# Kernel optimization log

Hardware: AMD Instinct MI355X
Metric: run time of the kernel (lower is better)

The kernel has to match this reference:

```python
import jax, jax.numpy as jnp
import numpy as np

N, E = 50000, 1600000
FEAT, HID, HEADS = 256, 64, 2
NEG_SLOPE = 0.2


def gat_conv(x, src, dst, W, att_src, att_dst, bias, heads, out_ch):
    """PyG GATConv (concat=True, self-loops already appended to src/dst)."""
    n = x.shape[0]
    h = (x @ W).reshape(n, heads, out_ch)                      # [N,H,C]
    a_src = jnp.einsum('nhc,hc->nh', h, att_src)               # [N,H]
    a_dst = jnp.einsum('nhc,hc->nh', h, att_dst)               # [N,H]
    alpha = jax.nn.leaky_relu(a_src[src] + a_dst[dst], NEG_SLOPE)  # [E',H]
    # segment softmax over incoming edges of each dst node
    amax = jax.ops.segment_max(alpha, dst, num_segments=n)
    alpha = jnp.exp(alpha - amax[dst])
    denom = jax.ops.segment_sum(alpha, dst, num_segments=n)
    alpha = alpha / (denom[dst] + 1e-16)
    msg = h[src] * alpha[..., None]                            # [E',H,C]
    out = jax.ops.segment_sum(msg, dst, num_segments=n)        # [N,H,C]
    return out.reshape(n, heads * out_ch) + bias


def setup_inputs() -> dict:
    key = jax.random.key(0)
    ks = jax.random.split(key, 10)
    x = jax.random.normal(ks[0], (N, FEAT), dtype=jnp.float32)
    edge_index = jax.random.randint(ks[1], (2, E), 0, N, dtype=jnp.int64)
    s1 = 1.0 / np.sqrt(FEAT)
    s2 = 1.0 / np.sqrt(HID * HEADS)
    sa = 1.0 / np.sqrt(HID)
    return {
        'x': x,
        'edge_index': edge_index,
        'W1': jax.random.uniform(ks[2], (FEAT, HEADS * HID), jnp.float32, -s1, s1),
        'att_src1': jax.random.uniform(ks[3], (HEADS, HID), jnp.float32, -sa, sa),
        'att_dst1': jax.random.uniform(ks[4], (HEADS, HID), jnp.float32, -sa, sa),
        'b1': jnp.zeros((HEADS * HID,), jnp.float32),
        'W2': jax.random.uniform(ks[5], (HEADS * HID, HID), jnp.float32, -s2, s2),
        'att_src2': jax.random.uniform(ks[6], (1, HID), jnp.float32, -sa, sa),
        'att_dst2': jax.random.uniform(ks[7], (1, HID), jnp.float32, -sa, sa),
        'b2': jnp.zeros((HID,), jnp.float32),
    }


def reference(x, edge_index, W1, att_src1, att_dst1, b1, W2, att_src2, att_dst2, b2):
    n = x.shape[0]
    loop = jnp.arange(n, dtype=edge_index.dtype)
    src = jnp.concatenate([edge_index[0], loop])   # add self loops (PyG default)
    dst = jnp.concatenate([edge_index[1], loop])
    h = gat_conv(x, src, dst, W1, att_src1, att_dst1, b1, HEADS, HID)
    h = jax.nn.relu(h)  # dropout is identity in eval mode
    h = gat_conv(h, src, dst, W2, att_src2, att_dst2, b2, 1, HID)
    return jax.nn.log_softmax(h, axis=1)
```

## Files before the change

kernel.cpp:

```cpp
#include <hip/hip_runtime.h>
#include <hip/hip_bf16.h>
#include <math.h>

typedef short bf16x8 __attribute__((ext_vector_type(8)));
typedef float f32x4 __attribute__((ext_vector_type(4)));

#define BSHIFT 7
#define BWIDTH 128
#define PCHUNK 8192

__global__ void prep_kernel(int* __restrict__ bcnt,
                            const float* __restrict__ W1, const float* __restrict__ W2,
                            __hip_bfloat16* __restrict__ W1t,
                            __hip_bfloat16* __restrict__ W2t) {
    if (blockIdx.x == 0) {
        bcnt[threadIdx.x] = 0;
        bcnt[threadIdx.x + 256] = 0;
        return;
    }
    int idx = (blockIdx.x - 1) * 256 + threadIdx.x;
    const int n1 = 128 * 256;
    if (idx < n1) {
        int nn = idx >> 8, kk = idx & 255;
        W1t[idx] = __float2bfloat16(W1[kk * 128 + nn]);
    } else {
        int j = idx - n1;
        if (j < 64 * 128) {
            int nn = j >> 7, kk = j & 127;
            W2t[j] = __float2bfloat16(W2[kk * 64 + nn]);
        }
    }
}

__global__ __launch_bounds__(256) void bucket_hist(const int* __restrict__ ei, int E,
                                                   int* __restrict__ bcnt) {
    __shared__ int h[512];
    int tid = threadIdx.x;
    for (int i = tid; i < 512; i += 256) h[i] = 0;
    __syncthreads();
    int start = blockIdx.x * PCHUNK;
    int cnt = min(PCHUNK, E - start);
    for (int i = tid; i < cnt; i += 256)
        atomicAdd(&h[ei[E + start + i] >> BSHIFT], 1);
    __syncthreads();
    for (int i = tid; i < 512; i += 256)
        if (h[i]) atomicAdd(&bcnt[i], h[i]);
}

__global__ __launch_bounds__(512) void bucket_scan(const int* __restrict__ bcnt,
                                                   int* __restrict__ bbase,
                                                   int* __restrict__ bcur,
                                                   int nbk, int n) {
    __shared__ int s[512];
    int tid = threadIdx.x;
    int nodes = 0;
    if (tid < nbk) nodes = min(BWIDTH, n - (tid << BSHIFT));
    int v = (tid < nbk) ? bcnt[tid] + nodes : 0;
    s[tid] = v;
    __syncthreads();
    #pragma unroll
    for (int o = 1; o < 512; o <<= 1) {
        int t = (tid >= o) ? s[tid - o] : 0;
        __syncthreads();
        s[tid] += t;
        __syncthreads();
    }
    if (tid < nbk) {
        int ex = s[tid] - v;
        bbase[tid] = ex;
        bcur[tid] = ex - (tid << BSHIFT);
    }
    if (tid == nbk) bbase[nbk] = s[tid];
}

__global__ __launch_bounds__(256) void partition_edges(const int* __restrict__ ei, int E,
                                                       int* __restrict__ bcur,
                                                       int* __restrict__ tmp) {
    __shared__ int stage[PCHUNK];
    __shared__ int h[512];
    __shared__ int lbase[512];
    int tid = threadIdx.x;
    int start = blockIdx.x * PCHUNK;
    int cnt = min(PCHUNK, E - start);
    for (int i = tid; i < 512; i += 256) h[i] = 0;
    __syncthreads();
    for (int i = tid; i < cnt; i += 256) {
        int s = ei[start + i];
        int d = ei[E + start + i];
        stage[i] = (s << 16) | d;
        atomicAdd(&h[d >> BSHIFT], 1);
    }
    __syncthreads();
    for (int i = tid; i < 512; i += 256) {
        if (h[i] > 0) lbase[i] = atomicAdd(&bcur[i], h[i]);
        h[i] = 0;
    }
    __syncthreads();
    for (int i = tid; i < cnt; i += 256) {
        int e = stage[i];
        int b = (e & 0xffff) >> BSHIFT;
        int r = atomicAdd(&h[b], 1);
        tmp[lbase[b] + r] = e;
    }
}

__global__ __launch_bounds__(256) void bucket_csr(const int* __restrict__ bbase,
                                                  const int* __restrict__ tmp,
                                                  int* __restrict__ offs,
                                                  int* __restrict__ srcs,
                                                  int n, int nbk) {
    __shared__ int cnt[BWIDTH];
    __shared__ int sa[BWIDTH];
    __shared__ int cur[BWIDTH];
    int b = blockIdx.x;
    int tid = threadIdx.x;
    int node0 = b << BSHIFT;
    int nnodes = min(BWIDTH, n - node0);
    int cb = bbase[b];
    int ce = bbase[b + 1];
    int tb = cb - node0;
    int ecnt = (ce - cb) - nnodes;

    if (tid < BWIDTH) cnt[tid] = (tid < nnodes) ? 1 : 0;
    __syncthreads();
    for (int i = tid; i < ecnt; i += 256)
        atomicAdd(&cnt[tmp[tb + i] & (BWIDTH - 1)], 1);
    __syncthreads();
    if (tid < BWIDTH) sa[tid] = cnt[tid];
    __syncthreads();
    #pragma unroll
    for (int o = 1; o < BWIDTH; o <<= 1) {
        int v = 0;
        if (tid < BWIDTH) { v = sa[tid]; if (tid >= o) v += sa[tid - o]; }
        __syncthreads();
        if (tid < BWIDTH) sa[tid] = v;
        __syncthreads();
    }
    if (tid < BWIDTH) {
        int ex = sa[tid] - cnt[tid];
        if (tid < nnodes) {
            offs[node0 + tid] = cb + ex;
            srcs[cb + ex] = node0 + tid;
        }
        cur[tid] = ex + (tid < nnodes ? 1 : 0);
    }
    if (b == nbk - 1 && tid == 0) offs[n] = ce;
    __syncthreads();
    for (int i = tid; i < ecnt; i += 256) {
        int e = tmp[tb + i];
        int li = e & (BWIDTH - 1);
        int r = atomicAdd(&cur[li], 1);
        srcs[cb + r] = ((unsigned)e) >> 16;
    }
}

template <bool A_BF16, int NT, int HEADS>
__global__ __launch_bounds__(256) void gemm_att(
    const void* __restrict__ Av, const __hip_bfloat16* __restrict__ Bt,
    __hip_bfloat16* __restrict__ C,
    const float* __restrict__ atts, const float* __restrict__ attd,
    float* __restrict__ a_s, float* __restrict__ a_d, int M, int K) {
    constexpr int N = NT * 16;
    __shared__ __hip_bfloat16 As[64][40];
    int tid = threadIdx.x;
    int w = tid >> 6, l = tid & 63;
    int q = l >> 4, m16 = l & 15;
    int bm = blockIdx.x * 64;

    int lr = tid >> 2, lseg = tid & 3;
    int arow = bm + lr; if (arow >= M) arow = M - 1;

    f32x4 acc[NT];
    #pragma unroll
    for (int t = 0; t < NT; t++) acc[t] = (f32x4){0.f, 0.f, 0.f, 0.f};

    for (int kc = 0; kc < K; kc += 32) {
        if (A_BF16) {
            const __hip_bfloat16* A = (const __hip_bfloat16*)Av;
            uint4 v = *(const uint4*)(A + (size_t)arow * K + kc + lseg * 8);
            *(uint4*)&As[lr][lseg * 8] = v;
        } else {
            const float* A = (const float*)Av;
            float4 v0 = *(const float4*)(A + (size_t)arow * K + kc + lseg * 8);
            float4 v1 = *(const float4*)(A + (size_t)arow * K + kc + lseg * 8 + 4);
            union { __hip_bfloat16 h[8]; uint4 u; } tmp;
            tmp.h[0] = __float2bfloat16(v0.x); tmp.h[1] = __float2bfloat16(v0.y);
            tmp.h[2] = __float2bfloat16(v0.z); tmp.h[3] = __float2bfloat16(v0.w);
            tmp.h[4] = __float2bfloat16(v1.x); tmp.h[5] = __float2bfloat16(v1.y);
            tmp.h[6] = __float2bfloat16(v1.z); tmp.h[7] = __float2bfloat16(v1.w);
            *(uint4*)&As[lr][lseg * 8] = tmp.u;
        }
        __syncthreads();
        bf16x8 a = *(const bf16x8*)&As[w * 16 + m16][q * 8];
        #pragma unroll
        for (int t = 0; t < NT; t++) {
            bf16x8 b = *(const bf16x8*)(Bt + (size_t)(t * 16 + m16) * K + kc + q * 8);
            acc[t] = __builtin_amdgcn_mfma_f32_16x16x32_bf16(a, b, acc[t], 0, 0, 0);
        }
        __syncthreads();
    }

    #pragma unroll
    for (int t = 0; t < NT; t++) {
        #pragma unroll
        for (int r = 0; r < 4; r++) {
            int row = bm + w * 16 + q * 4 + r;
            if (row < M) C[(size_t)row * N + t * 16 + m16] = __float2bfloat16(acc[t][r]);
        }
    }

    float ps[HEADS][4], pd[HEADS][4];
    #pragma unroll
    for (int hh = 0; hh < HEADS; hh++)
        #pragma unroll
        for (int r = 0; r < 4; r++) { ps[hh][r] = 0.f; pd[hh][r] = 0.f; }
    #pragma unroll
    for (int t = 0; t < NT; t++) {
        int ch = t * 16 + m16;
        float asw = atts[ch], adw = attd[ch];
        int hh = (HEADS == 2) ? (t >> 2) : 0;
        #pragma unroll
        for (int r = 0; r < 4; r++) {
            ps[hh][r] = fmaf(acc[t][r], asw, ps[hh][r]);
            pd[hh][r] = fmaf(acc[t][r], adw, pd[hh][r]);
        }
    }
    #pragma unroll
    for (int o = 1; o < 16; o <<= 1) {
        #pragma unroll
        for (int hh = 0; hh < HEADS; hh++)
            #pragma unroll
            for (int r = 0; r < 4; r++) {
                ps[hh][r] += __shfl_xor(ps[hh][r], o);
                pd[hh][r] += __shfl_xor(pd[hh][r], o);
            }
    }
    if (m16 == 0) {
        #pragma unroll
        for (int r = 0; r < 4; r++) {
            int row = bm + w * 16 + q * 4 + r;
            if (row < M) {
                if (HEADS == 2) {
                    a_s[row * 2]     = ps[0][r];
                    a_s[row * 2 + 1] = ps[1][r];
                    a_d[row * 2]     = pd[0][r];
                    a_d[row * 2 + 1] = pd[1][r];
                } else {
                    a_s[row] = ps[0][r];
                    a_d[row] = pd[0][r];
                }
            }
        }
    }
}

__device__ __forceinline__ float leaky(float r) {
    return r < 0.f ? 0.2f * r : r;
}

__device__ __forceinline__ void unpack2(unsigned u, float& lo, float& hi) {
    lo = __uint_as_float(u << 16);
    hi = __uint_as_float(u & 0xffff0000u);
}

__global__ __launch_bounds__(256) void edge_agg_l1(
    const int* __restrict__ offs, const int* __restrict__ srcs,
    const __hip_bfloat16* __restrict__ h1, const float* __restrict__ asv,
    const float* __restrict__ adv, const float* __restrict__ bias,
    __hip_bfloat16* __restrict__ out, int n) {
    int d = (blockIdx.x * blockDim.x + threadIdx.x) >> 6;
    int lane = threadIdx.x & 63;
    if (d >= n) return;
    int start = offs[d], end = offs[d + 1];
    float ad0 = adv[2 * d], ad1 = adv[2 * d + 1];

    int sub = lane & 15;
    int g = lane >> 4;
    int ch0 = sub * 8;
    int hsel = sub >> 3;

    float s0 = 0.f, s1 = 0.f;
    float acc[8];
    #pragma unroll
    for (int k = 0; k < 8; k++) acc[k] = 0.f;

    for (int base = start; base < end; base += 64) {
        int cnt = min(64, end - base);
        int s_l = 0;
        float e0 = 0.f, e1 = 0.f;
        if (lane < cnt) {
            s_l = srcs[base + lane];
            float2 a = *(const float2*)(asv + 2 * s_l);
            e0 = __expf(leaky(a.x + ad0));
            e1 = __expf(leaky(a.y + ad1));
        }
        s0 += e0;
        s1 += e1;

        int steps = (cnt + 3) >> 2;
        int jj = 0;
        for (; jj + 2 <= steps; jj += 2) {
            int eA = jj * 4 + g, eB = eA + 4;
            float w0A = __shfl(e0, eA), w1A = __shfl(e1, eA);
            int sA = __shfl(s_l, eA);
            float w0B = __shfl(e0, eB), w1B = __shfl(e1, eB);
            int sB = __shfl(s_l, eB);
            float wA = hsel ? w1A : w0A;
            float wB = hsel ? w1B : w0B;
            uint4 vA = *(const uint4*)(h1 + (size_t)sA * 128 + ch0);
            uint4 vB = *(const uint4*)(h1 + (size_t)sB * 128 + ch0);
            float f0, f1, f2, f3, f4, f5, f6, f7;
            unpack2(vA.x, f0, f1); unpack2(vA.y, f2, f3);
            unpack2(vA.z, f4, f5); unpack2(vA.w, f6, f7);
            acc[0] = fmaf(wA, f0, acc[0]); acc[1] = fmaf(wA, f1, acc[1]);
            acc[2] = fmaf(wA, f2, acc[2]); acc[3] = fmaf(wA, f3, acc[3]);
            acc[4] = fmaf(wA, f4, acc[4]); acc[5] = fmaf(wA, f5, acc[5]);
            acc[6] = fmaf(wA, f6, acc[6]); acc[7] = fmaf(wA, f7, acc[7]);
            unpack2(vB.x, f0, f1); unpack2(vB.y, f2, f3);
            unpack2(vB.z, f4, f5); unpack2(vB.w, f6, f7);
            acc[0] = fmaf(wB, f0, acc[0]); acc[1] = fmaf(wB, f1, acc[1]);
            acc[2] = fmaf(wB, f2, acc[2]); acc[3] = fmaf(wB, f3, acc[3]);
            acc[4] = fmaf(wB, f4, acc[4]); acc[5] = fmaf(wB, f5, acc[5]);
            acc[6] = fmaf(wB, f6, acc[6]); acc[7] = fmaf(wB, f7, acc[7]);
        }
        if (jj < steps) {
            int eA = jj * 4 + g;
            float w0A = __shfl(e0, eA), w1A = __shfl(e1, eA);
            int sA = __shfl(s_l, eA);
            float wA = hsel ? w1A : w0A;
            uint4 vA = *(const uint4*)(h1 + (size_t)sA * 128 + ch0);
            float f0, f1, f2, f3, f4, f5, f6, f7;
            unpack2(vA.x, f0, f1); unpack2(vA.y, f2, f3);
            unpack2(vA.z, f4, f5); unpack2(vA.w, f6, f7);
            acc[0] = fmaf(wA, f0, acc[0]); acc[1] = fmaf(wA, f1, acc[1]);
            acc[2] = fmaf(wA, f2, acc[2]); acc[3] = fmaf(wA, f3, acc[3]);
            acc[4] = fmaf(wA, f4, acc[4]); acc[5] = fmaf(wA, f5, acc[5]);
            acc[6] = fmaf(wA, f6, acc[6]); acc[7] = fmaf(wA, f7, acc[7]);
        }
    }
    #pragma unroll
    for (int o = 16; o < 64; o <<= 1)
        #pragma unroll
        for (int k = 0; k < 8; k++) acc[k] += __shfl_xor(acc[k], o);
    #pragma unroll
    for (int o = 1; o < 64; o <<= 1) {
        s0 += __shfl_xor(s0, o);
        s1 += __shfl_xor(s1, o);
    }

    if (lane < 16) {
        float invh = 1.f / ((hsel ? s1 : s0) + 1e-16f);
        float4 b0 = *(const float4*)(bias + ch0);
        float4 b1 = *(const float4*)(bias + ch0 + 4);
        union { __hip_bfloat16 h[8]; uint4 u; } o2;
        o2.h[0] = __float2bfloat16(fmaxf(fmaf(acc[0], invh, b0.x), 0.f));
        o2.h[1] = __float2bfloat16(fmaxf(fmaf(acc[1], invh, b0.y), 0.f));
        o2.h[2] = __float2bfloat16(fmaxf(fmaf(acc[2], invh, b0.z), 0.f));
        o2.h[3] = __float2bfloat16(fmaxf(fmaf(acc[3], invh, b0.w), 0.f));
        o2.h[4] = __float2bfloat16(fmaxf(fmaf(acc[4], invh, b1.x), 0.f));
        o2.h[5] = __float2bfloat16(fmaxf(fmaf(acc[5], invh, b1.y), 0.f));
        o2.h[6] = __float2bfloat16(fmaxf(fmaf(acc[6], invh, b1.z), 0.f));
        o2.h[7] = __float2bfloat16(fmaxf(fmaf(acc[7], invh, b1.w), 0.f));
        *(uint4*)(out + (size_t)d * 128 + ch0) = o2.u;
    }
}

__global__ __launch_bounds__(256) void edge_agg_l2(
    const int* __restrict__ offs, const int* __restrict__ srcs,
    const __hip_bfloat16* __restrict__ h2, const float* __restrict__ asv,
    const float* __restrict__ adv, const float* __restrict__ bias,
    float* __restrict__ out, int n) {
    int d = (blockIdx.x * blockDim.x + threadIdx.x) >> 6;
    int lane = threadIdx.x & 63;
    if (d >= n) return;
    int start = offs[d], end = offs[d + 1];
    float ad = adv[d];

    int sub = lane & 7;
    int g = lane >> 3;
    int ch0 = sub * 8;

    float ssum = 0.f;
    float acc[8];
    #pragma unroll
    for (int k = 0; k < 8; k++) acc[k] = 0.f;

    for (int base = start; base < end; base += 64) {
        int cnt = min(64, end - base);
        int s_l = 0;
        float ew = 0.f;
        if (lane < cnt) {
            s_l = srcs[base + lane];
            ew = __expf(leaky(asv[s_l] + ad));
        }
        ssum += ew;

        int steps = (cnt + 7) >> 3;
        int jj = 0;
        for (; jj + 2 <= steps; jj += 2) {
            int eA = jj * 8 + g, eB = eA + 8;
            float wA = __shfl(ew, eA);
            int sA = __shfl(s_l, eA);
            float wB = __shfl(ew, eB);
            int sB = __shfl(s_l, eB);
            uint4 vA = *(const uint4*)(h2 + (size_t)sA * 64 + ch0);
            uint4 vB = *(const uint4*)(h2 + (size_t)sB * 64 + ch0);
            float f0, f1, f2, f3, f4, f5, f6, f7;
            unpack2(vA.x, f0, f1); unpack2(vA.y, f2, f3);
            unpack2(vA.z, f4, f5); unpack2(vA.w, f6, f7);
            acc[0] = fmaf(wA, f0, acc[0]); acc[1] = fmaf(wA, f1, acc[1]);
            acc[2] = fmaf(wA, f2, acc[2]); acc[3] = fmaf(wA, f3, acc[3]);
            acc[4] = fmaf(wA, f4, acc[4]); acc[5] = fmaf(wA, f5, acc[5]);
            acc[6] = fmaf(wA, f6, acc[6]); acc[7] = fmaf(wA, f7, acc[7]);
            unpack2(vB.x, f0, f1); unpack2(vB.y, f2, f3);
            unpack2(vB.z, f4, f5); unpack2(vB.w, f6, f7);
            acc[0] = fmaf(wB, f0, acc[0]); acc[1] = fmaf(wB, f1, acc[1]);
            acc[2] = fmaf(wB, f2, acc[2]); acc[3] = fmaf(wB, f3, acc[3]);
            acc[4] = fmaf(wB, f4, acc[4]); acc[5] = fmaf(wB, f5, acc[5]);
            acc[6] = fmaf(wB, f6, acc[6]); acc[7] = fmaf(wB, f7, acc[7]);
        }
        if (jj < steps) {
            int eA = jj * 8 + g;
            float wA = __shfl(ew, eA);
            int sA = __shfl(s_l, eA);
            uint4 vA = *(const uint4*)(h2 + (size_t)sA * 64 + ch0);
            float f0, f1, f2, f3, f4, f5, f6, f7;
            unpack2(vA.x, f0, f1); unpack2(vA.y, f2, f3);
            unpack2(vA.z, f4, f5); unpack2(vA.w, f6, f7);
            acc[0] = fmaf(wA, f0, acc[0]); acc[1] = fmaf(wA, f1, acc[1]);
            acc[2] = fmaf(wA, f2, acc[2]); acc[3] = fmaf(wA, f3, acc[3]);
            acc[4] = fmaf(wA, f4, acc[4]); acc[5] = fmaf(wA, f5, acc[5]);
            acc[6] = fmaf(wA, f6, acc[6]); acc[7] = fmaf(wA, f7, acc[7]);
        }
    }
    #pragma unroll
    for (int o = 8; o < 64; o <<= 1)
        #pragma unroll
        for (int k = 0; k < 8; k++) acc[k] += __shfl_xor(acc[k], o);
    #pragma unroll
    for (int o = 1; o < 64; o <<= 1) ssum += __shfl_xor(ssum, o);

    float inv = 1.f / (ssum + 1e-16f);
    float4 b0 = *(const float4*)(bias + ch0);
    float4 b1 = *(const float4*)(bias + ch0 + 4);
    float v[8];
    v[0] = fmaf(acc[0], inv, b0.x); v[1] = fmaf(acc[1], inv, b0.y);
    v[2] = fmaf(acc[2], inv, b0.z); v[3] = fmaf(acc[3], inv, b0.w);
    v[4] = fmaf(acc[4], inv, b1.x); v[5] = fmaf(acc[5], inv, b1.y);
    v[6] = fmaf(acc[6], inv, b1.z); v[7] = fmaf(acc[7], inv, b1.w);

    float vm = v[0];
    #pragma unroll
    for (int k = 1; k < 8; k++) vm = fmaxf(vm, v[k]);
    #pragma unroll
    for (int o = 1; o < 8; o <<= 1) vm = fmaxf(vm, __shfl_xor(vm, o));
    float se_loc = 0.f;
    #pragma unroll
    for (int k = 0; k < 8; k++) se_loc += __expf(v[k] - vm);
    #pragma unroll
    for (int o = 1; o < 8; o <<= 1) se_loc += __shfl_xor(se_loc, o);
    float lse = vm + logf(se_loc);

    if (lane < 8) {
        float4 o0 = make_float4(v[0] - lse, v[1] - lse, v[2] - lse, v[3] - lse);
        float4 o1 = make_float4(v[4] - lse, v[5] - lse, v[6] - lse, v[7] - lse);
        *(float4*)(out + (size_t)d * 64 + ch0) = o0;
        *(float4*)(out + (size_t)d * 64 + ch0 + 4) = o1;
    }
}

extern "C" void kernel_launch(void* const* d_in, const int* in_sizes, int n_in,
                              void* d_out, int out_size, void* d_ws, size_t ws_size,
                              hipStream_t stream) {
    const float* x    = (const float*)d_in[0];
    const int*   ei   = (const int*)d_in[1];
    const float* W1   = (const float*)d_in[2];
    const float* as1w = (const float*)d_in[3];
    const float* ad1w = (const float*)d_in[4];
    const float* b1   = (const float*)d_in[5];
    const float* W2   = (const float*)d_in[6];
    const float* as2w = (const float*)d_in[7];
    const float* ad2w = (const float*)d_in[8];
    const float* b2   = (const float*)d_in[9];
    float* out = (float*)d_out;

    const int n = in_sizes[0] / 256;
    const int E = in_sizes[1] / 2;
    const int tot = E + n;
    const int nbk = (n + BWIDTH - 1) / BWIDTH;

    char* p = (char*)d_ws;
    auto alloc = [&](size_t bytes) {
        void* r = (void*)p;
        p += (bytes + 255) & ~(size_t)255;
        return r;
    };
    int*   offs  = (int*)alloc((size_t)(n + 1) * 4);
    int*   srcs  = (int*)alloc((size_t)tot * 4);
    int*   tmp   = (int*)alloc((size_t)E * 4);
    int*   bcnt  = (int*)alloc(512 * 4);
    int*   bbase = (int*)alloc(512 * 4);
    int*   bcur  = (int*)alloc(512 * 4);
    __hip_bfloat16* W1t = (__hip_bfloat16*)alloc((size_t)128 * 256 * 2);
    __hip_bfloat16* W2t = (__hip_bfloat16*)alloc((size_t)64 * 128 * 2);
    __hip_bfloat16* h1  = (__hip_bfloat16*)alloc((size_t)n * 128 * 2);
    __hip_bfloat16* out1= (__hip_bfloat16*)alloc((size_t)n * 128 * 2);
    __hip_bfloat16* h2  = (__hip_bfloat16*)alloc((size_t)n * 64 * 2);
    float* a_s1 = (float*)alloc((size_t)n * 2 * 4);
    float* a_d1 = (float*)alloc((size_t)n * 2 * 4);
    float* a_s2 = (float*)alloc((size_t)n * 4);
    float* a_d2 = (float*)alloc((size_t)n * 4);

    int pblocks = (E + PCHUNK - 1) / PCHUNK;

    prep_kernel<<<1 + (128 * 256 + 64 * 128 + 255) / 256, 256, 0, stream>>>(
        bcnt, W1, W2, W1t, W2t);

    bucket_hist<<<pblocks, 256, 0, stream>>>(ei, E, bcnt);
    bucket_scan<<<1, 512, 0, stream>>>(bcnt, bbase, bcur, nbk, n);
    partition_edges<<<pblocks, 256, 0, stream>>>(ei, E, bcur, tmp);
    bucket_csr<<<nbk, 256, 0, stream>>>(bbase, tmp, offs, srcs, n, nbk);

    gemm_att<false, 8, 2><<<(n + 63) / 64, 256, 0, stream>>>(
        x, W1t, h1, as1w, ad1w, a_s1, a_d1, n, 256);
    edge_agg_l1<<<((size_t)n * 64 + 255) / 256, 256, 0, stream>>>(
        offs, srcs, h1, a_s1, a_d1, b1, out1, n);

    gemm_att<true, 4, 1><<<(n + 63) / 64, 256, 0, stream>>>(
        out1, W2t, h2, as2w, ad2w, a_s2, a_d2, n, 128);
    edge_agg_l2<<<((size_t)n * 64 + 255) / 256, 256, 0, stream>>>(
        offs, srcs, h2, a_s2, a_d2, b2, out, n);
}
```

Before: 286.5 us.

## Fuse CSR build pipeline into one cooperative kernel with grid syncs

Replaces the prep, histogram, scan, partition and per-bucket CSR kernels with a single cooperative kernel separated by grid.sync barriers. Each block stages its edge chunk in LDS once and reuses it for both the histogram and the partition phases, so edges are read from global memory only once. Every block redundantly computes the bucket scan, and the weight transpose is folded into the same kernel. PCHUNK is halved so the grid covers both edges and buckets, with launch bounds chosen so all blocks stay co-resident. The cost is grid-wide barrier latency and a dependence on co-residency for the cooperative launch.

New measurement: 435.6 us. +52.0%, slower.

```diff
diff --git a/kernel.cpp b/kernel.cpp
--- a/kernel.cpp
+++ b/kernel.cpp
@@ -1,156 +1,142 @@
 #include <hip/hip_runtime.h>
 #include <hip/hip_bf16.h>
+#include <hip/hip_cooperative_groups.h>
 #include <math.h>
+
+namespace cg = cooperative_groups;
 
 typedef short bf16x8 __attribute__((ext_vector_type(8)));
 typedef float f32x4 __attribute__((ext_vector_type(4)));
 
 #define BSHIFT 7
 #define BWIDTH 128
-#define PCHUNK 8192
-
-__global__ void prep_kernel(int* __restrict__ bcnt,
-                            const float* __restrict__ W1, const float* __restrict__ W2,
-                            __hip_bfloat16* __restrict__ W1t,
-                            __hip_bfloat16* __restrict__ W2t) {
-    if (blockIdx.x == 0) {
-        bcnt[threadIdx.x] = 0;
-        bcnt[threadIdx.x + 256] = 0;
-        return;
-    }
-    int idx = (blockIdx.x - 1) * 256 + threadIdx.x;
-    const int n1 = 128 * 256;
-    if (idx < n1) {
-        int nn = idx >> 8, kk = idx & 255;
-        W1t[idx] = __float2bfloat16(W1[kk * 128 + nn]);
-    } else {
-        int j = idx - n1;
-        if (j < 64 * 128) {
-            int nn = j >> 7, kk = j & 127;
-            W2t[j] = __float2bfloat16(W2[kk * 64 + nn]);
-        }
-    }
-}
-
-__global__ __launch_bounds__(256) void bucket_hist(const int* __restrict__ ei, int E,
-                                                   int* __restrict__ bcnt) {
+#define PCHUNK 4096
+
+__global__ __launch_bounds__(256, 2) void build_coop(
+    const int* __restrict__ ei, int E,
+    const float* __restrict__ W1, const float* __restrict__ W2,
+    __hip_bfloat16* __restrict__ W1t, __hip_bfloat16* __restrict__ W2t,
+    int* __restrict__ bcnt, int* __restrict__ bcur, int* __restrict__ tmp,
+    int* __restrict__ offs, int* __restrict__ srcs, int n, int nbk) {
+    cg::grid_group grid = cg::this_grid();
+    __shared__ int stage[PCHUNK];
     __shared__ int h[512];
-    int tid = threadIdx.x;
+    __shared__ int aux[512];
+    __shared__ int bb[513];
+    int b = blockIdx.x, tid = threadIdx.x;
+    int nblk = gridDim.x;
+
     for (int i = tid; i < 512; i += 256) h[i] = 0;
     __syncthreads();
-    int start = blockIdx.x * PCHUNK;
-    int cnt = min(PCHUNK, E - start);
-    for (int i = tid; i < cnt; i += 256)
-        atomicAdd(&h[ei[E + start + i] >> BSHIFT], 1);
-    __syncthreads();
-    for (int i = tid; i < 512; i += 256)
-        if (h[i]) atomicAdd(&bcnt[i], h[i]);
-}
-
-__global__ __launch_bounds__(512) void bucket_scan(const int* __restrict__ bcnt,
-                                                   int* __restrict__ bbase,
-                                                   int* __restrict__ bcur,
-                                                   int nbk, int n) {
-    __shared__ int s[512];
-    int tid = threadIdx.x;
-    int nodes = 0;
-    if (tid < nbk) nodes = min(BWIDTH, n - (tid << BSHIFT));
-    int v = (tid < nbk) ? bcnt[tid] + nodes : 0;
-    s[tid] = v;
-    __syncthreads();
-    #pragma unroll
-    for (int o = 1; o < 512; o <<= 1) {
-        int t = (tid >= o) ? s[tid - o] : 0;
-        __syncthreads();
-        s[tid] += t;
-        __syncthreads();
-    }
-    if (tid < nbk) {
-        int ex = s[tid] - v;
-        bbase[tid] = ex;
-        bcur[tid] = ex - (tid << BSHIFT);
-    }
-    if (tid == nbk) bbase[nbk] = s[tid];
-}
-
-__global__ __launch_bounds__(256) void partition_edges(const int* __restrict__ ei, int E,
-                                                       int* __restrict__ bcur,
-                                                       int* __restrict__ tmp) {
-    __shared__ int stage[PCHUNK];
-    __shared__ int h[512];
-    __shared__ int lbase[512];
-    int tid = threadIdx.x;
-    int start = blockIdx.x * PCHUNK;
-    int cnt = min(PCHUNK, E - start);
-    for (int i = tid; i < 512; i += 256) h[i] = 0;
-    __syncthreads();
+    int start = b * PCHUNK;
+    int cnt = E - start;
+    cnt = cnt < 0 ? 0 : (cnt > PCHUNK ? PCHUNK : cnt);
     for (int i = tid; i < cnt; i += 256) {
         int s = ei[start + i];
         int d = ei[E + start + i];
         stage[i] = (s << 16) | d;
         atomicAdd(&h[d >> BSHIFT], 1);
     }
+    {
+        const int TW = 128 * 256 + 64 * 128;
+        for (int idx = b * 256 + tid; idx < TW; idx += nblk * 256) {
+            if (idx < 128 * 256) {
+                int nn = idx >> 8, kk = idx & 255;
+                W1t[idx] = __float2bfloat16(W1[kk * 128 + nn]);
+            } else {
+                int j = idx - 128 * 256;
+                int nn = j >> 7, kk = j & 127;
+                W2t[j] = __float2bfloat16(W2[kk * 64 + nn]);
+            }
+        }
+    }
     __syncthreads();
-    for (int i = tid; i < 512; i += 256) {
-        if (h[i] > 0) lbase[i] = atomicAdd(&bcur[i], h[i]);
-        h[i] = 0;
-    }
-    __syncthreads();
-    for (int i = tid; i < cnt; i += 256) {
-        int e = stage[i];
-        int b = (e & 0xffff) >> BSHIFT;
-        int r = atomicAdd(&h[b], 1);
-        tmp[lbase[b] + r] = e;
-    }
-}
-
-__global__ __launch_bounds__(256) void bucket_csr(const int* __restrict__ bbase,
-                                                  const int* __restrict__ tmp,
-                                                  int* __restrict__ offs,
-                                                  int* __restrict__ srcs,
-                                                  int n, int nbk) {
-    __shared__ int cnt[BWIDTH];
-    __shared__ int sa[BWIDTH];
-    __shared__ int cur[BWIDTH];
-    int b = blockIdx.x;
-    int tid = threadIdx.x;
-    int node0 = b << BSHIFT;
-    int nnodes = min(BWIDTH, n - node0);
-    int cb = bbase[b];
-    int ce = bbase[b + 1];
-    int tb = cb - node0;
-    int ecnt = (ce - cb) - nnodes;
-
-    if (tid < BWIDTH) cnt[tid] = (tid < nnodes) ? 1 : 0;
-    __syncthreads();
-    for (int i = tid; i < ecnt; i += 256)
-        atomicAdd(&cnt[tmp[tb + i] & (BWIDTH - 1)], 1);
-    __syncthreads();
-    if (tid < BWIDTH) sa[tid] = cnt[tid];
-    __syncthreads();
-    #pragma unroll
-    for (int o = 1; o < BWIDTH; o <<= 1) {
-        int v = 0;
-        if (tid < BWIDTH) { v = sa[tid]; if (tid >= o) v += sa[tid - o]; }
-        __syncthreads();
-        if (tid < BWIDTH) sa[tid] = v;
-        __syncthreads();
-    }
-    if (tid < BWIDTH) {
-        int ex = sa[tid] - cnt[tid];
-        if (tid < nnodes) {
-            offs[node0 + tid] = cb + ex;
-            srcs[cb + ex] = node0 + tid;
-        }
-        cur[tid] = ex + (tid < nnodes ? 1 : 0);
-    }
-    if (b == nbk - 1 && tid == 0) offs[n] = ce;
-    __syncthreads();
-    for (int i = tid; i < ecnt; i += 256) {
-        int e = tmp[tb + i];
-        int li = e & (BWIDTH - 1);
-        int r = atomicAdd(&cur[li], 1);
-        srcs[cb + r] = ((unsigned)e) >> 16;
+    for (int i = tid; i < 512; i += 256)
+        if (h[i]) atomicAdd(&bcnt[i], h[i]);
+    grid.sync();
+
+    {
+        int j0 = 2 * tid, j1 = 2 * tid + 1;
+        int nodes0 = (j0 < nbk) ? min(BWIDTH, n - (j0 << BSHIFT)) : 0;
+        int nodes1 = (j1 < nbk) ? min(BWIDTH, n - (j1 << BSHIFT)) : 0;
+        int v0 = bcnt[j0] + nodes0;
+        int v1 = bcnt[j1] + nodes1;
+        int psum = v0 + v1;
+        aux[tid] = psum;
+        __syncthreads();
+        #pragma unroll
+        for (int o = 1; o < 256; o <<= 1) {
+            int add = (tid >= o) ? aux[tid - o] : 0;
+            __syncthreads();
+            aux[tid] += add;
+            __syncthreads();
+        }
+        int incl = aux[tid];
+        int excl = incl - psum;
+        bb[j0] = excl;
+        bb[j1] = excl + v0;
+        if (tid == 255) bb[512] = incl;
+        __syncthreads();
+        if (tid == 0 && b < nbk) bcur[b] = bb[b] - (b << BSHIFT);
+        if (b == nbk - 1 && tid == 0) offs[n] = bb[nbk];
+    }
+    grid.sync();
+
+    {
+        for (int i = tid; i < 512; i += 256) {
+            int c = h[i];
+            aux[i] = (c > 0) ? atomicAdd(&bcur[i], c) : 0;
+            h[i] = 0;
+        }
+        __syncthreads();
+        for (int i = tid; i < cnt; i += 256) {
+            int e = stage[i];
+            int bkt = (e & 0xffff) >> BSHIFT;
+            int r = atomicAdd(&h[bkt], 1);
+            tmp[aux[bkt] + r] = e;
+        }
+    }
+    grid.sync();
+
+    if (b < nbk) {
+        int* cnt128 = h;
+        int* sa = h + 128;
+        int* cur = h + 256;
+        int node0 = b << BSHIFT;
+        int nnodes = min(BWIDTH, n - node0);
+        int cb = bb[b], ce = bb[b + 1];
+        int tb = cb - node0;
+        int ecnt = (ce - cb) - nnodes;
+        if (tid < BWIDTH) cnt128[tid] = (tid < nnodes) ? 1 : 0;
+        __syncthreads();
+        for (int i = tid; i < ecnt; i += 256)
+            atomicAdd(&cnt128[tmp[tb + i] & (BWIDTH - 1)], 1);
+        __syncthreads();
+        if (tid < BWIDTH) sa[tid] = cnt128[tid];
+        __syncthreads();
+        #pragma unroll
+        for (int o = 1; o < BWIDTH; o <<= 1) {
+            int v = 0;
+            if (tid < BWIDTH) { v = sa[tid]; if (tid >= o) v += sa[tid - o]; }
+            __syncthreads();
+            if (tid < BWIDTH) sa[tid] = v;
+            __syncthreads();
+        }
+        if (tid < BWIDTH) {
+            int ex = sa[tid] - cnt128[tid];
+            if (tid < nnodes) {
+                offs[node0 + tid] = cb + ex;
+                srcs[cb + ex] = node0 + tid;
+            }
+            cur[tid] = ex + (tid < nnodes ? 1 : 0);
+        }
+        __syncthreads();
+        for (int i = tid; i < ecnt; i += 256) {
+            int e = tmp[tb + i];
+            int li = e & (BWIDTH - 1);
+            int r = atomicAdd(&cur[li], 1);
+            srcs[cb + r] = ((unsigned)e) >> 16;
+        }
     }
 }
 
@@ -484,10 +470,12 @@
     const float* b2   = (const float*)d_in[9];
     float* out = (float*)d_out;
 
-    const int n = in_sizes[0] / 256;
-    const int E = in_sizes[1] / 2;
+    int n = in_sizes[0] / 256;
+    int E = in_sizes[1] / 2;
     const int tot = E + n;
-    const int nbk = (n + BWIDTH - 1) / BWIDTH;
+    int nbk = (n + BWIDTH - 1) / BWIDTH;
+    int pblocks = (E + PCHUNK - 1) / PCHUNK;
+    int gblocks = pblocks > nbk ? pblocks : nbk;
 
     char* p = (char*)d_ws;
     auto alloc = [&](size_t bytes) {
@@ -499,7 +487,6 @@
     int*   srcs  = (int*)alloc((size_t)tot * 4);
     int*   tmp   = (int*)alloc((size_t)E * 4);
     int*   bcnt  = (int*)alloc(512 * 4);
-    int*   bbase = (int*)alloc(512 * 4);
     int*   bcur  = (int*)alloc(512 * 4);
     __hip_bfloat16* W1t = (__hip_bfloat16*)alloc((size_t)128 * 256 * 2);
     __hip_bfloat16* W2t = (__hip_bfloat16*)alloc((size_t)64 * 128 * 2);
@@ -511,15 +498,15 @@
     float* a_s2 = (float*)alloc((size_t)n * 4);
     float* a_d2 = (float*)alloc((size_t)n * 4);
 
-    int pblocks = (E + PCHUNK - 1) / PCHUNK;
-
-    prep_kernel<<<1 + (128 * 256 + 64 * 128 + 255) / 256, 256, 0, stream>>>(
-        bcnt, W1, W2, W1t, W2t);
-
-    bucket_hist<<<pblocks, 256, 0, stream>>>(ei, E, bcnt);
-    bucket_scan<<<1, 512, 0, stream>>>(bcnt, bbase, bcur, nbk, n);
-    partition_edges<<<pblocks, 256, 0, stream>>>(ei, E, bcur, tmp);
-    bucket_csr<<<nbk, 256, 0, stream>>>(bbase, tmp, offs, srcs, n, nbk);
+    hipMemsetAsync(bcnt, 0, 512 * 4, stream);
+    {
+        void* args[] = {
+            (void*)&ei, (void*)&E, (void*)&W1, (void*)&W2,
+            (void*)&W1t, (void*)&W2t, (void*)&bcnt, (void*)&bcur,
+            (void*)&tmp, (void*)&offs, (void*)&srcs, (void*)&n, (void*)&nbk};
+        hipLaunchCooperativeKernel((void*)build_coop, dim3(gblocks), dim3(256),
+                                   args, 0, stream);
+    }
 
     gemm_att<false, 8, 2><<<(n + 63) / 64, 256, 0, stream>>>(
         x, W1t, h1, as1w, ad1w, a_s1, a_d1, n, 256);
```
